# Performance work log

Hardware: AMD Instinct MI355X
Metric: run time of the kernel (lower is better)

## Reference

```python
import jax, jax.numpy as jnp
import numpy as np

B, N, DIM = 4, 1024, 1024
HEADS, DH = 16, 64
INNER = HEADS * DH          # 1024
PROJ_H = max(16, DH // 8)   # 16
TOP_K = 256
TEMP = 1.0
SCALE = DH ** -0.5
LN_EPS = 1e-5


def setup_inputs() -> dict:
    key = jax.random.key(0)
    ks = jax.random.split(key, 9)
    s = 0.02
    return {
        "x": jax.random.normal(ks[0], (B, N, DIM), dtype=jnp.float32),
        "w_qkv": jax.random.normal(ks[1], (3 * INNER, DIM), dtype=jnp.float32) * s,
        "w_out": jax.random.normal(ks[2], (DIM, INNER), dtype=jnp.float32) * s,
        "b_out": jnp.zeros((DIM,), dtype=jnp.float32),
        "ln_g": jnp.ones((DH,), dtype=jnp.float32),
        "ln_b": jnp.zeros((DH,), dtype=jnp.float32),
        "w1": jax.random.normal(ks[3], (PROJ_H, DH), dtype=jnp.float32) * s,
        "b1": jnp.zeros((PROJ_H,), dtype=jnp.float32),
        "w2": jax.random.normal(ks[4], (1, PROJ_H), dtype=jnp.float32) * s,
        "b2": jnp.zeros((1,), dtype=jnp.float32),
    }


def _soma_gate(token_feat, ln_g, ln_b, w1, b1, w2, b2):
    # token_feat: [B, N, DH] -> gate [B, N] in (0,1)
    mu = token_feat.mean(axis=-1, keepdims=True)
    var = token_feat.var(axis=-1, keepdims=True)
    H = (token_feat - mu) * jax.lax.rsqrt(var + LN_EPS) * ln_g + ln_b
    h = jax.nn.gelu(H @ w1.T + b1, approximate=False)
    scores = (h @ w2.T + b2)[..., 0]                       # [B, N]
    scores = scores / (TEMP + 1e-12)
    # top-k soft mask: non-topk positions set to -1e9 before sigmoid
    topk_vals, topk_idx = jax.lax.top_k(scores, TOP_K)
    b_idx = jnp.arange(scores.shape[0])[:, None]
    scores = jnp.full_like(scores, -1e9).at[b_idx, topk_idx].set(topk_vals)
    return jax.nn.sigmoid(scores)


def reference(x, w_qkv, w_out, b_out, ln_g, ln_b, w1, b1, w2, b2):
    Bx, Nx, _ = x.shape
    qkv = x @ w_qkv.T                                      # [B, N, 3*INNER]
    q, k, v = jnp.split(qkv, 3, axis=-1)
    to_heads = lambda t: t.reshape(Bx, Nx, HEADS, DH).transpose(0, 2, 1, 3)
    q, k, v = to_heads(q), to_heads(k), to_heads(v)        # [B, H, N, DH]

    dots = jnp.einsum('bhid,bhjd->bhij', q, k) * SCALE     # [B, H, N, N]

    q_mean = q.mean(axis=1)                                # [B, N, DH]
    gate = _soma_gate(q_mean, ln_g, ln_b, w1, b1, w2, b2)  # [B, N]
    dots = dots * (gate[:, None, :, None] * gate[:, None, None, :])

    attn = jax.nn.softmax(dots, axis=-1)
    out = jnp.einsum('bhij,bhjd->bhid', attn, v)           # [B, H, N, DH]
    out = out.transpose(0, 2, 1, 3).reshape(Bx, Nx, INNER)
    return out @ w_out.T + b_out
```

## Files before the change

### kernel.cpp

```cpp
#include <hip/hip_runtime.h>
#include <hip/hip_bf16.h>
#include <stdint.h>

typedef __bf16 bf16;
typedef __bf16 bf16x8 __attribute__((ext_vector_type(8)));
typedef float floatx4 __attribute__((ext_vector_type(4)));

typedef const __attribute__((address_space(1))) uint32_t glb_u32;
typedef __attribute__((address_space(3))) uint32_t lds_u32;

__device__ __forceinline__ void cp16(void* lds, const void* gp) {
    __builtin_amdgcn_global_load_lds((glb_u32*)gp, (lds_u32*)lds, 16, 0, 0);
}

#define MFMA16(a, b, c) __builtin_amdgcn_mfma_f32_16x16x32_bf16((a), (b), (c), 0, 0, 0)
#define SCALE_ 0.125f

__global__ __launch_bounds__(256) void k_cvt_prep(
    const float* __restrict__ x, const float* __restrict__ wq,
    const float* __restrict__ wo, bf16* __restrict__ xb,
    bf16* __restrict__ xl, bf16* __restrict__ wqb, bf16* __restrict__ wob,
    bf16* __restrict__ whl) {
    if (blockIdx.x < 4096) {
        size_t i8 = ((size_t)blockIdx.x * 256 + threadIdx.x) * 8;
        const float* src; bf16* dst; size_t off; bool isx = false;
        if (i8 < 4194304)      { src = x;  dst = xb;  off = i8; isx = true; }
        else if (i8 < 7340032) { src = wq; dst = wqb; off = i8 - 4194304; }
        else                   { src = wo; dst = wob; off = i8 - 7340032; }
        float4 a = *(const float4*)(src + off);
        float4 b = *(const float4*)(src + off + 4);
        union { bf16 h[8]; uint4 u; } hi, lo;
        hi.h[0] = (bf16)a.x; hi.h[1] = (bf16)a.y; hi.h[2] = (bf16)a.z; hi.h[3] = (bf16)a.w;
        hi.h[4] = (bf16)b.x; hi.h[5] = (bf16)b.y; hi.h[6] = (bf16)b.z; hi.h[7] = (bf16)b.w;
        *(uint4*)(dst + off) = hi.u;
        if (isx) {
            lo.h[0] = (bf16)(a.x - (float)hi.h[0]);
            lo.h[1] = (bf16)(a.y - (float)hi.h[1]);
            lo.h[2] = (bf16)(a.z - (float)hi.h[2]);
            lo.h[3] = (bf16)(a.w - (float)hi.h[3]);
            lo.h[4] = (bf16)(b.x - (float)hi.h[4]);
            lo.h[5] = (bf16)(b.y - (float)hi.h[5]);
            lo.h[6] = (bf16)(b.z - (float)hi.h[6]);
            lo.h[7] = (bf16)(b.w - (float)hi.h[7]);
            *(uint4*)(xl + off) = lo.u;
        }
    } else {
        int t = (blockIdx.x - 4096) * 256 + threadIdx.x;
        int k = t & 1023, d = t >> 10;
        float s = 0.f;
        #pragma unroll
        for (int h = 0; h < 16; ++h) s += wq[(size_t)(h * 64 + d) * 1024 + k];
        s *= (1.f / 16.f);
        bf16 hi = (bf16)s;
        whl[(size_t)d * 1024 + k] = hi;
        whl[(size_t)(64 + d) * 1024 + k] = (bf16)(s - (float)hi);
    }
}

__global__ __launch_bounds__(256) void k_score_gemm(
    const bf16* __restrict__ xh, const bf16* __restrict__ xl,
    const bf16* __restrict__ whl, float* __restrict__ qmbuf) {
    __shared__ bf16 Ah[128 * 32];
    __shared__ bf16 Al[128 * 32];
    __shared__ bf16 Bs[128 * 32];
    const int t = threadIdx.x;
    const int lane = t & 63;
    const int w = t >> 6;
    const int m0 = blockIdx.x * 128;
    const int srow = t >> 2;
    const int scol = (t & 3) * 8;
    const int fr = lane & 15;
    const int kc = (lane >> 4) * 8;
    const int wm0 = w * 32;

    floatx4 zero4 = {0.f, 0.f, 0.f, 0.f};
    floatx4 acc[2][4];
    #pragma unroll
    for (int i = 0; i < 2; ++i)
        #pragma unroll
        for (int j = 0; j < 4; ++j) acc[i][j] = zero4;

    for (int k0 = 0; k0 < 1024; k0 += 32) {
        __syncthreads();
        cp16(Ah + t * 8,        xh + (size_t)(m0 + srow) * 1024 + k0 + scol);
        cp16(Ah + t * 8 + 2048, xh + (size_t)(m0 + srow + 64) * 1024 + k0 + scol);
        cp16(Al + t * 8,        xl + (size_t)(m0 + srow) * 1024 + k0 + scol);
        cp16(Al + t * 8 + 2048, xl + (size_t)(m0 + srow + 64) * 1024 + k0 + scol);
        cp16(Bs + t * 8,        whl + (size_t)srow * 1024 + k0 + scol);
        cp16(Bs + t * 8 + 2048, whl + (size_t)(srow + 64) * 1024 + k0 + scol);
        __syncthreads();
        bf16x8 ah[2], al[2], bh[4], bl[4];
        #pragma unroll
        for (int mi = 0; mi < 2; ++mi) {
            ah[mi] = *(const bf16x8*)&Ah[(wm0 + mi * 16 + fr) * 32 + kc];
            al[mi] = *(const bf16x8*)&Al[(wm0 + mi * 16 + fr) * 32 + kc];
        }
        #pragma unroll
        for (int ni = 0; ni < 4; ++ni) {
            bh[ni] = *(const bf16x8*)&Bs[(ni * 16 + fr) * 32 + kc];
            bl[ni] = *(const bf16x8*)&Bs[(64 + ni * 16 + fr) * 32 + kc];
        }
        #pragma unroll
        for (int mi = 0; mi < 2; ++mi)
            #pragma unroll
            for (int ni = 0; ni < 4; ++ni) {
                acc[mi][ni] = MFMA16(ah[mi], bh[ni], acc[mi][ni]);
                acc[mi][ni] = MFMA16(ah[mi], bl[ni], acc[mi][ni]);
                acc[mi][ni] = MFMA16(al[mi], bh[ni], acc[mi][ni]);
            }
    }

    const int rowb = (lane >> 4) * 4;
    #pragma unroll
    for (int mi = 0; mi < 2; ++mi)
        #pragma unroll
        for (int ni = 0; ni < 4; ++ni)
            #pragma unroll
            for (int r = 0; r < 4; ++r) {
                const int row = m0 + wm0 + mi * 16 + rowb + r;
                qmbuf[(size_t)row * 64 + ni * 16 + fr] = acc[mi][ni][r];
            }
}

__global__ __launch_bounds__(256) void k_score_tail(
    const float* __restrict__ qmbuf, const float* __restrict__ lng,
    const float* __restrict__ lnb, const float* __restrict__ w1f,
    const float* __restrict__ b1f, const float* __restrict__ w2f,
    const float* __restrict__ b2f, float* __restrict__ scores) {
    const int w = threadIdx.x >> 6, lane = threadIdx.x & 63;
    const int r = blockIdx.x * 4 + w;
    __shared__ float Hs[4][64];
    __shared__ float hh[4][16];

    float qm = qmbuf[(size_t)r * 64 + lane];
    float s = qm;
    #pragma unroll
    for (int off = 32; off > 0; off >>= 1) s += __shfl_xor(s, off);
    float mu = s * (1.f / 64.f);
    float dx = qm - mu;
    float v2 = dx * dx;
    #pragma unroll
    for (int off = 32; off > 0; off >>= 1) v2 += __shfl_xor(v2, off);
    float var = v2 * (1.f / 64.f);
    float H = dx * (1.0f / sqrtf(var + 1e-5f)) * lng[lane] + lnb[lane];
    Hs[w][lane] = H;
    if (lane < 16) {
        float a = b1f[lane];
        #pragma unroll
        for (int d = 0; d < 64; ++d) a += Hs[w][d] * w1f[lane * 64 + d];
        hh[w][lane] = 0.5f * a * (1.0f + erff(a * 0.70710678118654752f));
    }
    if (lane == 0) {
        float sc = b2f[0];
        #pragma unroll
        for (int p = 0; p < 16; ++p) sc += hh[w][p] * w2f[p];
        scores[r] = sc;
    }
}

__global__ __launch_bounds__(256) void k_topk(const float* __restrict__ scores,
                                              float* __restrict__ gate,
                                              int* __restrict__ idx,
                                              float* __restrict__ gsel) {
    const int w = threadIdx.x >> 6, lane = threadIdx.x & 63;
    const float* sc = scores + w * 1024;
    float s[16];
    uint32_t key[16];
    #pragma unroll
    for (int i = 0; i < 16; ++i) {
        s[i] = sc[lane * 16 + i];
        uint32_t u = __float_as_uint(s[i]);
        key[i] = (u >> 31) ? ~u : (u | 0x80000000u);
    }
    uint32_t prefix = 0;
    for (int bit = 31; bit >= 0; --bit) {
        uint32_t cand = prefix | (1u << bit);
        int c = 0;
        #pragma unroll
        for (int i = 0; i < 16; ++i) c += (key[i] >= cand);
        #pragma unroll
        for (int off = 1; off < 64; off <<= 1) c += __shfl_xor(c, off);
        if (c >= 256) prefix = cand;
    }
    int cg = 0, eq = 0;
    #pragma unroll
    for (int i = 0; i < 16; ++i) { cg += (key[i] > prefix); eq += (key[i] == prefix); }
    #pragma unroll
    for (int off = 1; off < 64; off <<= 1) cg += __shfl_xor(cg, off);
    const int quota = 256 - cg;
    int xs = eq;
    #pragma unroll
    for (int off = 1; off < 64; off <<= 1) {
        int y = __shfl_up(xs, off);
        if (lane >= off) xs += y;
    }
    int run = xs - eq;
    bool selv[16];
    int cnt = 0;
    #pragma unroll
    for (int i = 0; i < 16; ++i) {
        bool sel = key[i] > prefix;
        if (key[i] == prefix) { sel = (run < quota); run++; }
        selv[i] = sel;
        cnt += sel ? 1 : 0;
        gate[w * 1024 + lane * 16 + i] = sel ? 1.0f / (1.0f + expf(-s[i])) : 0.0f;
    }
    int xc = cnt;
    #pragma unroll
    for (int off = 1; off < 64; off <<= 1) {
        int y = __shfl_up(xc, off);
        if (lane >= off) xc += y;
    }
    int pos = xc - cnt;
    #pragma unroll
    for (int i = 0; i < 16; ++i) {
        if (selv[i]) {
            idx[w * 256 + pos]  = lane * 16 + i;
            gsel[w * 256 + pos] = 1.0f / (1.0f + expf(-s[i]));
            pos++;
        }
    }
}

__global__ __launch_bounds__(256) void k_xsum(const bf16* __restrict__ xb,
                                              float* __restrict__ xsum4) {
    const int i = blockIdx.x;
    const int nq = i & 3, b = (i >> 2) & 3, c0 = (i >> 4) << 6;
    const int lane = threadIdx.x & 63, q = threadIdx.x >> 6;
    __shared__ float red[4][64];
    const bf16* p = xb + (size_t)b * 1048576 +
                    (size_t)(nq * 256 + q * 64) * 1024 + c0 + lane;
    float s = 0.f;
    #pragma unroll 8
    for (int n = 0; n < 64; ++n) s += (float)p[(size_t)n * 1024];
    red[q][lane] = s;
    __syncthreads();
    if (threadIdx.x < 64)
        xsum4[((size_t)nq * 4 + b) * 1024 + c0 + threadIdx.x] =
            red[0][threadIdx.x] + red[1][threadIdx.x] +
            red[2][threadIdx.x] + red[3][threadIdx.x];
}

__global__ __launch_bounds__(256) void k_qkv_sel(
    const bf16* __restrict__ xb, const bf16* __restrict__ wqb,
    const int* __restrict__ idx, bf16* __restrict__ qsel,
    bf16* __restrict__ ksel, bf16* __restrict__ VselT) {
    __shared__ bf16 As[128 * 32];
    __shared__ bf16 Bs[128 * 32];
    const int t = threadIdx.x;
    const int lane = t & 63;
    const int w = t >> 6;
    const int srow = t >> 2;
    const int scol = (t & 3) * 8;
    const int wm = (w & 1) * 64;
    const int wn = (w >> 1) * 64;
    const int fr = lane & 15;
    const int kc = (lane >> 4) * 8;

    const int bid = blockIdx.x;
    const int n0 = (bid % 24) * 128;
    const int m0 = (bid / 24) * 128;
    const bf16* Bsrc = wqb + (size_t)n0 * 1024;
    const int mg1 = m0 + srow, mg2 = mg1 + 64;
    const int tok1 = idx[(mg1 >> 8) * 256 + (mg1 & 255)];
    const int tok2 = idx[(mg2 >> 8) * 256 + (mg2 & 255)];
    const size_t abase1 = ((size_t)(mg1 >> 8) * 1024 + tok1) * 1024;
    const size_t abase2 = ((size_t)(mg2 >> 8) * 1024 + tok2) * 1024;

    floatx4 zero4 = {0.f, 0.f, 0.f, 0.f};
    floatx4 acc[4][4];
    #pragma unroll
    for (int i = 0; i < 4; ++i)
        #pragma unroll
        for (int j = 0; j < 4; ++j) acc[i][j] = zero4;

    for (int k0 = 0; k0 < 1024; k0 += 32) {
        __syncthreads();
        cp16(As + t * 8,        xb + abase1 + k0 + scol);
        cp16(As + t * 8 + 2048, xb + abase2 + k0 + scol);
        cp16(Bs + t * 8,        Bsrc + (size_t)srow * 1024 + k0 + scol);
        cp16(Bs + t * 8 + 2048, Bsrc + (size_t)(srow + 64) * 1024 + k0 + scol);
        __syncthreads();
        bf16x8 a[4], b[4];
        #pragma unroll
        for (int mi = 0; mi < 4; ++mi)
            a[mi] = *(const bf16x8*)&As[(wm + mi * 16 + fr) * 32 + kc];
        #pragma unroll
        for (int ni = 0; ni < 4; ++ni)
            b[ni] = *(const bf16x8*)&Bs[(wn + ni * 16 + fr) * 32 + kc];
        #pragma unroll
        for (int mi = 0; mi < 4; ++mi)
            #pragma unroll
            for (int ni = 0; ni < 4; ++ni)
                acc[mi][ni] = MFMA16(a[mi], b[ni], acc[mi][ni]);
    }

    const int rowb = (lane >> 4) * 4;
    #pragma unroll
    for (int ni = 0; ni < 4; ++ni) {
        const int n_base = n0 + wn + ni * 16;
        const int region = n_base >> 10;
        const int nn = n_base & 1023;
        const int h = nn >> 6;
        const int dd = (nn & 63) + fr;
        if (region < 2) {
            #pragma unroll
            for (int mi = 0; mi < 4; ++mi)
                #pragma unroll
                for (int r = 0; r < 4; ++r) {
                    const int mg = m0 + wm + mi * 16 + rowb + r;
                    const bf16 v = (bf16)acc[mi][ni][r];
                    if (region == 0) {
                        qsel[(size_t)mg * 1024 + h * 64 + dd] = v;
                    } else {
                        const int b = mg >> 8, s = mg & 255;
                        ksel[(((size_t)(b * 16 + h)) * 256 + s) * 64 + dd] = v;
                    }
                }
        } else {
            #pragma unroll
            for (int mi = 0; mi < 4; ++mi) {
                const int mgb = m0 + wm + mi * 16 + rowb;
                const int b = mgb >> 8, s0 = mgb & 255;
                union { bf16 h4[4]; uint2 u; } pk;
                #pragma unroll
                for (int r = 0; r < 4; ++r) pk.h4[r] = (bf16)acc[mi][ni][r];
                *(uint2*)&VselT[(((size_t)(b * 16 + h)) * 64 + dd) * 256 + s0] = pk.u;
            }
        }
    }
}

__global__ __launch_bounds__(256) void k_sumv(
    const float* __restrict__ xsum4, const bf16* __restrict__ wqb,
    const bf16* __restrict__ VselT, float* __restrict__ SumVuns,
    bf16* __restrict__ qsel) {
    const int bh = blockIdx.x, b = bh >> 4, h = bh & 15;
    const int t = threadIdx.x, d = t & 63, part = t >> 6;
    __shared__ float xs[1024];
    __shared__ float redA[4][64];
    __shared__ float redS[4][64];

    for (int k = t; k < 1024; k += 256)
        xs[k] = xsum4[(size_t)(0 * 4 + b) * 1024 + k] +
                xsum4[(size_t)(1 * 4 + b) * 1024 + k] +
                xsum4[(size_t)(2 * 4 + b) * 1024 + k] +
                xsum4[(size_t)(3 * 4 + b) * 1024 + k];
    __syncthreads();

    const bf16* wrow = wqb + (size_t)(2048 + h * 64 + d) * 1024 + part * 256;
    float sa = 0.f;
    #pragma unroll
    for (int k = 0; k < 256; k += 8) {
        bf16x8 v = *(const bf16x8*)(wrow + k);
        #pragma unroll
        for (int j = 0; j < 8; ++j) sa += (float)v[j] * xs[part * 256 + k + j];
    }
    redA[part][d] = sa;

    const bf16* vrow = VselT + (size_t)bh * 16384 + (size_t)d * 256 + part * 64;
    float ss = 0.f;
    #pragma unroll
    for (int k = 0; k < 64; k += 8) {
        bf16x8 v = *(const bf16x8*)(vrow + k);
        #pragma unroll
        for (int j = 0; j < 8; ++j) ss += (float)v[j];
    }
    redS[part][d] = ss;
    __syncthreads();

    if (t < 64) {
        float sA = redA[0][t] + redA[1][t] + redA[2][t] + redA[3][t];
        float sS = redS[0][t] + redS[1][t] + redS[2][t] + redS[3][t];
        SumVuns[bh * 64 + t] = sA - sS;
        qsel[(size_t)(1024 + b) * 1024 + h * 64 + t] = (bf16)(sA * (1.f / 1024.f));
    }
}

__global__ __launch_bounds__(256) void k_attn(
    bf16* __restrict__ qsel, const bf16* __restrict__ Ksel,
    const bf16* __restrict__ VselT, const float* __restrict__ gsel,
    const float* __restrict__ SumVuns) {
    const int bh = blockIdx.x;
    const int qt = blockIdx.y;
    const int b = bh >> 4, h = bh & 15;
    const int t = threadIdx.x, w = t >> 6, lane = t & 63;
    const int m0 = qt * 64;
    const bf16* kb = Ksel + (size_t)bh * 16384;
    const bf16* vb = VselT + (size_t)bh * 16384;

    __shared__ bf16 Qs[64 * 72];
    __shared__ bf16 Ks[64 * 72];
    __shared__ bf16 Vs[64 * 72];
    __shared__ bf16 Ps[4][16 * 72];

    #pragma unroll
    for (int c = 0; c < 2; ++c) {
        int idx2 = t + 256 * c, row = idx2 >> 3, c8 = (idx2 & 7) * 8;
        *(uint4*)&Qs[row * 72 + c8] =
            *(const uint4*)&qsel[(size_t)(b * 256 + m0 + row) * 1024 + h * 64 + c8];
    }
    const int fr = lane & 15;
    const int kq = lane >> 4;
    const int rowb = kq * 4;
    __syncthreads();
    bf16x8 aq[2];
    aq[0] = *(const bf16x8*)&Qs[(w * 16 + fr) * 72 + kq * 8];
    aq[1] = *(const bf16x8*)&Qs[(w * 16 + fr) * 72 + 32 + kq * 8];

    float gq[4];
    #pragma unroll
    for (int r = 0; r < 4; ++r)
        gq[r] = gsel[b * 256 + m0 + w * 16 + rowb + r] * SCALE_;

    float mrow[4] = {0.f, 0.f, 0.f, 0.f};
    float lrow[4] = {0.f, 0.f, 0.f, 0.f};
    floatx4 zero4 = {0.f, 0.f, 0.f, 0.f};
    floatx4 Of[4] = {zero4, zero4, zero4, zero4};

    for (int jt = 0; jt < 4; ++jt) {
        const int j0 = jt * 64;
        __syncthreads();
        #pragma unroll
        for (int c = 0; c < 2; ++c) {
            int idx2 = t + 256 * c, row = idx2 >> 3, c8 = (idx2 & 7) * 8;
            *(uint4*)&Ks[row * 72 + c8] = *(const uint4*)&kb[(size_t)(j0 + row) * 64 + c8];
            *(uint4*)&Vs[row * 72 + c8] = *(const uint4*)&vb[(size_t)row * 256 + j0 + c8];
        }
        __syncthreads();

        floatx4 S[4] = {zero4, zero4, zero4, zero4};
        #pragma unroll
        for (int ks = 0; ks < 2; ++ks) {
            #pragma unroll
            for (int ni = 0; ni < 4; ++ni) {
                bf16x8 bfr = *(const bf16x8*)&Ks[(ni * 16 + fr) * 72 + ks * 32 + kq * 8];
                S[ni] = MFMA16(aq[ks], bfr, S[ni]);
            }
        }
        float gk[4];
        #pragma unroll
        for (int ni = 0; ni < 4; ++ni) gk[ni] = gsel[b * 256 + j0 + ni * 16 + fr];

        float p[4][4], rmax[4] = {0.f, 0.f, 0.f, 0.f};
        #pragma unroll
        for (int ni = 0; ni < 4; ++ni)
            #pragma unroll
            for (int r = 0; r < 4; ++r) {
                float sv = S[ni][r] * (gq[r] * gk[ni]);
                p[ni][r] = sv;
                rmax[r] = fmaxf(rmax[r], sv);
            }
        #pragma unroll
        for (int r = 0; r < 4; ++r) {
            #pragma unroll
            for (int off = 1; off < 16; off <<= 1)
                rmax[r] = fmaxf(rmax[r], __shfl_xor(rmax[r], off));
        }
        float alpha[4], rsum[4] = {0.f, 0.f, 0.f, 0.f};
        #pragma unroll
        for (int r = 0; r < 4; ++r) {
            float mn = fmaxf(mrow[r], rmax[r]);
            alpha[r] = __expf(mrow[r] - mn);
            mrow[r] = mn;
        }
        #pragma unroll
        for (int ni = 0; ni < 4; ++ni)
            #pragma unroll
            for (int r = 0; r < 4; ++r) {
                float pv = __expf(p[ni][r] - mrow[r]);
                p[ni][r] = pv;
                rsum[r] += pv;
            }
        #pragma unroll
        for (int r = 0; r < 4; ++r) {
            #pragma unroll
            for (int off = 1; off < 16; off <<= 1) rsum[r] += __shfl_xor(rsum[r], off);
            lrow[r] = lrow[r] * alpha[r] + rsum[r];
        }
        #pragma unroll
        for (int nd = 0; nd < 4; ++nd)
            #pragma unroll
            for (int r = 0; r < 4; ++r) Of[nd][r] *= alpha[r];

        #pragma unroll
        for (int ni = 0; ni < 4; ++ni)
            #pragma unroll
            for (int r = 0; r < 4; ++r)
                Ps[w][(rowb + r) * 72 + ni * 16 + fr] = (bf16)p[ni][r];

        #pragma unroll
        for (int ks = 0; ks < 2; ++ks) {
            bf16x8 ap = *(const bf16x8*)&Ps[w][fr * 72 + ks * 32 + kq * 8];
            #pragma unroll
            for (int nd = 0; nd < 4; ++nd) {
                bf16x8 bv = *(const bf16x8*)&Vs[(nd * 16 + fr) * 72 + ks * 32 + kq * 8];
                Of[nd] = MFMA16(ap, bv, Of[nd]);
            }
        }
    }

    #pragma unroll
    for (int nd = 0; nd < 4; ++nd)
        #pragma unroll
        for (int r = 0; r < 4; ++r) {
            float em = __expf(-mrow[r]);
            float num = Of[nd][r] + em * SumVuns[bh * 64 + nd * 16 + fr];
            float den = lrow[r] + 768.0f * em;
            qsel[(size_t)(b * 256 + m0 + w * 16 + rowb + r) * 1024 +
                 h * 64 + nd * 16 + fr] = (bf16)(num / den);
        }
}

__global__ __launch_bounds__(256) void k_out_sel(
    const bf16* __restrict__ A, const bf16* __restrict__ wob,
    const float* __restrict__ b_out, const int* __restrict__ idx,
    float* __restrict__ ubase, float* __restrict__ out) {
    __shared__ bf16 As[128 * 32];
    __shared__ bf16 Bs[128 * 32];
    const int t = threadIdx.x;
    const int lane = t & 63;
    const int w = t >> 6;
    const int n0 = blockIdx.x * 128;
    const int m0 = blockIdx.y * 128;
    const bf16* Bsrc = wob + (size_t)n0 * 1024;

    const int srow = t >> 2;
    const int scol = (t & 3) * 8;
    const int wm = (w & 1) * 64;
    const int wn = (w >> 1) * 64;
    const int fr = lane & 15;
    const int kc = (lane >> 4) * 8;

    floatx4 zero4 = {0.f, 0.f, 0.f, 0.f};
    floatx4 acc[4][4];
    #pragma unroll
    for (int i = 0; i < 4; ++i)
        #pragma unroll
        for (int j = 0; j < 4; ++j) acc[i][j] = zero4;

    for (int k0 = 0; k0 < 1024; k0 += 32) {
        __syncthreads();
        cp16(As + t * 8,        A + (size_t)(m0 + srow) * 1024 + k0 + scol);
        cp16(As + t * 8 + 2048, A + (size_t)(m0 + srow + 64) * 1024 + k0 + scol);
        cp16(Bs + t * 8,        Bsrc + (size_t)srow * 1024 + k0 + scol);
        cp16(Bs + t * 8 + 2048, Bsrc + (size_t)(srow + 64) * 1024 + k0 + scol);
        __syncthreads();
        bf16x8 a[4], b[4];
        #pragma unroll
        for (int mi = 0; mi < 4; ++mi)
            a[mi] = *(const bf16x8*)&As[(wm + mi * 16 + fr) * 32 + kc];
        #pragma unroll
        for (int ni = 0; ni < 4; ++ni)
            b[ni] = *(const bf16x8*)&Bs[(wn + ni * 16 + fr) * 32 + kc];
        #pragma unroll
        for (int mi = 0; mi < 4; ++mi)
            #pragma unroll
            for (int ni = 0; ni < 4; ++ni)
                acc[mi][ni] = MFMA16(a[mi], b[ni], acc[mi][ni]);
    }

    const int rowb = (lane >> 4) * 4;
    #pragma unroll
    for (int ni = 0; ni < 4; ++ni) {
        const int ng = n0 + wn + ni * 16 + fr;
        const float bias = b_out[ng];
        #pragma unroll
        for (int mi = 0; mi < 4; ++mi)
            #pragma unroll
            for (int r = 0; r < 4; ++r) {
                const int mg = m0 + wm + mi * 16 + rowb + r;
                const float val = acc[mi][ni][r] + bias;
                if (mg < 1024) {
                    const int b = mg >> 8, s = mg & 255;
                    const int tok = idx[b * 256 + s];
                    out[((size_t)b * 1024 + tok) * 1024 + ng] = val;
                } else if (mg < 1028) {
                    ubase[(size_t)(mg - 1024) * 1024 + ng] = val;
                }
            }
    }
}

__global__ __launch_bounds__(256) void k_fill(
    const float* __restrict__ gate, const float* __restrict__ ubase,
    float* __restrict__ out) {
    const int tokg = blockIdx.x;
    if (gate[tokg] > 0.f) return;
    const int b = tokg >> 10;
    const int c = threadIdx.x * 4;
    *(float4*)(out + (size_t)tokg * 1024 + c) = *(const float4*)(ubase + b * 1024 + c);
}

extern "C" void kernel_launch(void* const* d_in, const int* in_sizes, int n_in,
                              void* d_out, int out_size, void* d_ws, size_t ws_size,
                              hipStream_t stream) {
    const float* x     = (const float*)d_in[0];
    const float* w_qkv = (const float*)d_in[1];
    const float* w_out = (const float*)d_in[2];
    const float* b_out = (const float*)d_in[3];
    const float* ln_g  = (const float*)d_in[4];
    const float* ln_b  = (const float*)d_in[5];
    const float* w1    = (const float*)d_in[6];
    const float* b1    = (const float*)d_in[7];
    const float* w2    = (const float*)d_in[8];
    const float* b2    = (const float*)d_in[9];
    float* out = (float*)d_out;

    char* ws = (char*)d_ws;
    bf16*  qsel  = (bf16*)(ws);
    bf16*  ksel  = (bf16*)(ws + 4194304);
    bf16*  VselT = (bf16*)(ws + 6291456);
    float* xsum4 = (float*)(ws + 8388608);
    bf16*  xb    = (bf16*)(ws + 16777216);
    bf16*  wqb   = (bf16*)(ws + 25165824);
    bf16*  wob   = (bf16*)(ws + 31457280);
    int*   idx     = (int*)(ws + 33554432);
    float* gsel    = (float*)(ws + 33558528);
    float* scores  = (float*)(ws + 33562624);
    float* gate    = (float*)(ws + 33579008);
    float* SumVuns = (float*)(ws + 33595392);
    float* ubase   = (float*)(ws + 33611776);
    bf16*  whl     = (bf16*)(ws + 33685504);
    float* qmbuf   = (float*)(ws + 34603008);
    bf16*  xlbuf   = (bf16*)(ws + 35651584);

    k_cvt_prep<<<4352, 256, 0, stream>>>(x, w_qkv, w_out, xb, xlbuf, wqb, wob, whl);
    k_xsum<<<256, 256, 0, stream>>>(xb, xsum4);
    k_score_gemm<<<32, 256, 0, stream>>>(xb, xlbuf, whl, qmbuf);
    k_score_tail<<<1024, 256, 0, stream>>>(qmbuf, ln_g, ln_b, w1, b1, w2, b2, scores);
    k_topk<<<1, 256, 0, stream>>>(scores, gate, idx, gsel);
    k_qkv_sel<<<192, 256, 0, stream>>>(xb, wqb, idx, qsel, ksel, VselT);
    k_sumv<<<64, 256, 0, stream>>>(xsum4, wqb, VselT, SumVuns, qsel);
    k_attn<<<dim3(64, 4), 256, 0, stream>>>(qsel, ksel, VselT, gsel, SumVuns);
    k_out_sel<<<dim3(8, 9), 256, 0, stream>>>(qsel, wob, b_out, idx, ubase, out);
    k_fill<<<4096, 256, 0, stream>>>(gate, ubase, out);
}
```

Baseline: 225.4 us.

## Fuse auxiliary kernels into neighbors to cut launch count from ten to six

Folds the column-sum of x into the conversion kernel, reading fp32 x directly. The score tail (LayerNorm, MLP, GELU) moves into the score GEMM epilogue through shared memory. The mean-V projection and the ubase output row become extra blocks inside the qkv and attention kernels, and the fill pass becomes extra blocks of the output GEMM. Intent is to remove launch and serialization overhead and intermediate buffer round-trips. In exchange the sum-over-V reduction is recomputed per attention block, and some blocks are unbalanced or sequential, such as the 32-row serial loop in the GEMM epilogue.

Result: slower. 240.1 us (+6.5%).

```diff
diff --git a/kernel.cpp b/kernel.cpp
--- a/kernel.cpp
+++ b/kernel.cpp
@@ -20,7 +20,8 @@
     const float* __restrict__ x, const float* __restrict__ wq,
     const float* __restrict__ wo, bf16* __restrict__ xb,
     bf16* __restrict__ xl, bf16* __restrict__ wqb, bf16* __restrict__ wob,
-    bf16* __restrict__ whl) {
+    bf16* __restrict__ whl, float* __restrict__ xsum) {
+    __shared__ float red[4][64];
     if (blockIdx.x < 4096) {
         size_t i8 = ((size_t)blockIdx.x * 256 + threadIdx.x) * 8;
         const float* src; bf16* dst; size_t off; bool isx = false;
@@ -44,7 +45,7 @@
             lo.h[7] = (bf16)(b.w - (float)hi.h[7]);
             *(uint4*)(xl + off) = lo.u;
         }
-    } else {
+    } else if (blockIdx.x < 4352) {
         int t = (blockIdx.x - 4096) * 256 + threadIdx.x;
         int k = t & 1023, d = t >> 10;
         float s = 0.f;
@@ -54,15 +55,34 @@
         bf16 hi = (bf16)s;
         whl[(size_t)d * 1024 + k] = hi;
         whl[(size_t)(64 + d) * 1024 + k] = (bf16)(s - (float)hi);
+    } else {
+        int j = blockIdx.x - 4352;
+        int b = j >> 4, c0 = (j & 15) << 6;
+        int lane = threadIdx.x & 63, q = threadIdx.x >> 6;
+        const float* p = x + (size_t)b * 1048576 + (size_t)q * 262144 + c0 + lane;
+        float s = 0.f;
+        #pragma unroll 8
+        for (int n = 0; n < 256; ++n) s += p[(size_t)n * 1024];
+        red[q][lane] = s;
+        __syncthreads();
+        if (threadIdx.x < 64)
+            xsum[b * 1024 + c0 + threadIdx.x] =
+                red[0][threadIdx.x] + red[1][threadIdx.x] +
+                red[2][threadIdx.x] + red[3][threadIdx.x];
     }
 }
 
 __global__ __launch_bounds__(256) void k_score_gemm(
     const bf16* __restrict__ xh, const bf16* __restrict__ xl,
-    const bf16* __restrict__ whl, float* __restrict__ qmbuf) {
+    const bf16* __restrict__ whl, const float* __restrict__ lng,
+    const float* __restrict__ lnb, const float* __restrict__ w1f,
+    const float* __restrict__ b1f, const float* __restrict__ w2f,
+    const float* __restrict__ b2f, float* __restrict__ scores) {
     __shared__ bf16 Ah[128 * 32];
     __shared__ bf16 Al[128 * 32];
     __shared__ bf16 Bs[128 * 32];
+    __shared__ float Sbuf[128][65];
+    __shared__ float Hs[4][64];
     const int t = threadIdx.x;
     const int lane = t & 63;
     const int w = t >> 6;
@@ -116,45 +136,41 @@
         #pragma unroll
         for (int ni = 0; ni < 4; ++ni)
             #pragma unroll
-            for (int r = 0; r < 4; ++r) {
-                const int row = m0 + wm0 + mi * 16 + rowb + r;
-                qmbuf[(size_t)row * 64 + ni * 16 + fr] = acc[mi][ni][r];
-            }
-}
-
-__global__ __launch_bounds__(256) void k_score_tail(
-    const float* __restrict__ qmbuf, const float* __restrict__ lng,
-    const float* __restrict__ lnb, const float* __restrict__ w1f,
-    const float* __restrict__ b1f, const float* __restrict__ w2f,
-    const float* __restrict__ b2f, float* __restrict__ scores) {
-    const int w = threadIdx.x >> 6, lane = threadIdx.x & 63;
-    const int r = blockIdx.x * 4 + w;
-    __shared__ float Hs[4][64];
-    __shared__ float hh[4][16];
-
-    float qm = qmbuf[(size_t)r * 64 + lane];
-    float s = qm;
-    #pragma unroll
-    for (int off = 32; off > 0; off >>= 1) s += __shfl_xor(s, off);
-    float mu = s * (1.f / 64.f);
-    float dx = qm - mu;
-    float v2 = dx * dx;
-    #pragma unroll
-    for (int off = 32; off > 0; off >>= 1) v2 += __shfl_xor(v2, off);
-    float var = v2 * (1.f / 64.f);
-    float H = dx * (1.0f / sqrtf(var + 1e-5f)) * lng[lane] + lnb[lane];
-    Hs[w][lane] = H;
-    if (lane < 16) {
-        float a = b1f[lane];
-        #pragma unroll
-        for (int d = 0; d < 64; ++d) a += Hs[w][d] * w1f[lane * 64 + d];
-        hh[w][lane] = 0.5f * a * (1.0f + erff(a * 0.70710678118654752f));
-    }
-    if (lane == 0) {
-        float sc = b2f[0];
-        #pragma unroll
-        for (int p = 0; p < 16; ++p) sc += hh[w][p] * w2f[p];
-        scores[r] = sc;
+            for (int r = 0; r < 4; ++r)
+                Sbuf[wm0 + mi * 16 + rowb + r][ni * 16 + fr] = acc[mi][ni][r];
+
+    const int p = lane & 15, q = lane >> 4;
+    float w1r[16];
+    #pragma unroll
+    for (int j = 0; j < 16; ++j) w1r[j] = w1f[p * 64 + q * 16 + j];
+    const float b1r = b1f[p], w2r = w2f[p], b2r = b2f[0];
+    const float lgr = lng[lane], lbr = lnb[lane];
+    __syncthreads();
+    for (int rr = 0; rr < 32; ++rr) {
+        const int row = w * 32 + rr;
+        float qm = Sbuf[row][lane];
+        float s = qm;
+        #pragma unroll
+        for (int off = 32; off > 0; off >>= 1) s += __shfl_xor(s, off);
+        float mu = s * (1.f / 64.f);
+        float dx = qm - mu;
+        float v2 = dx * dx;
+        #pragma unroll
+        for (int off = 32; off > 0; off >>= 1) v2 += __shfl_xor(v2, off);
+        float var = v2 * (1.f / 64.f);
+        float H = dx * (1.0f / sqrtf(var + 1e-5f)) * lgr + lbr;
+        Hs[w][lane] = H;
+        float pa = 0.f;
+        #pragma unroll
+        for (int j = 0; j < 16; ++j) pa += Hs[w][q * 16 + j] * w1r[j];
+        pa += __shfl_xor(pa, 16);
+        pa += __shfl_xor(pa, 32);
+        float a = pa + b1r;
+        float g = 0.5f * a * (1.0f + erff(a * 0.70710678118654752f));
+        float sc = g * w2r;
+        #pragma unroll
+        for (int off = 1; off < 16; off <<= 1) sc += __shfl_xor(sc, off);
+        if (lane == 0) scores[m0 + row] = sc + b2r;
     }
 }
 
@@ -222,32 +238,32 @@
     }
 }
 
-__global__ __launch_bounds__(256) void k_xsum(const bf16* __restrict__ xb,
-                                              float* __restrict__ xsum4) {
-    const int i = blockIdx.x;
-    const int nq = i & 3, b = (i >> 2) & 3, c0 = (i >> 4) << 6;
-    const int lane = threadIdx.x & 63, q = threadIdx.x >> 6;
-    __shared__ float red[4][64];
-    const bf16* p = xb + (size_t)b * 1048576 +
-                    (size_t)(nq * 256 + q * 64) * 1024 + c0 + lane;
-    float s = 0.f;
-    #pragma unroll 8
-    for (int n = 0; n < 64; ++n) s += (float)p[(size_t)n * 1024];
-    red[q][lane] = s;
-    __syncthreads();
-    if (threadIdx.x < 64)
-        xsum4[((size_t)nq * 4 + b) * 1024 + c0 + threadIdx.x] =
-            red[0][threadIdx.x] + red[1][threadIdx.x] +
-            red[2][threadIdx.x] + red[3][threadIdx.x];
-}
-
 __global__ __launch_bounds__(256) void k_qkv_sel(
     const bf16* __restrict__ xb, const bf16* __restrict__ wqb,
     const int* __restrict__ idx, bf16* __restrict__ qsel,
-    bf16* __restrict__ ksel, bf16* __restrict__ VselT) {
+    bf16* __restrict__ ksel, bf16* __restrict__ VselT,
+    const float* __restrict__ xsum, float* __restrict__ meanVbuf) {
     __shared__ bf16 As[128 * 32];
     __shared__ bf16 Bs[128 * 32];
+    __shared__ float xsS[1024];
     const int t = threadIdx.x;
+
+    if (blockIdx.x >= 192) {
+        const int j = blockIdx.x - 192, b = j >> 2, kq = j & 3;
+        for (int k = t; k < 1024; k += 256) xsS[k] = xsum[b * 1024 + k];
+        __syncthreads();
+        const int k2 = kq * 256 + t;
+        const bf16* wr = wqb + (size_t)(2048 + k2) * 1024;
+        float s = 0.f;
+        for (int k = 0; k < 1024; k += 8) {
+            bf16x8 v = *(const bf16x8*)(wr + k);
+            #pragma unroll
+            for (int jj = 0; jj < 8; ++jj) s += (float)v[jj] * xsS[k + jj];
+        }
+        meanVbuf[b * 1024 + k2] = s * (1.f / 1024.f);
+        return;
+    }
+
     const int lane = t & 63;
     const int w = t >> 6;
     const int srow = t >> 2;
@@ -331,68 +347,43 @@
     }
 }
 
-__global__ __launch_bounds__(256) void k_sumv(
-    const float* __restrict__ xsum4, const bf16* __restrict__ wqb,
-    const bf16* __restrict__ VselT, float* __restrict__ SumVuns,
-    bf16* __restrict__ qsel) {
-    const int bh = blockIdx.x, b = bh >> 4, h = bh & 15;
-    const int t = threadIdx.x, d = t & 63, part = t >> 6;
-    __shared__ float xs[1024];
-    __shared__ float redA[4][64];
-    __shared__ float redS[4][64];
-
-    for (int k = t; k < 1024; k += 256)
-        xs[k] = xsum4[(size_t)(0 * 4 + b) * 1024 + k] +
-                xsum4[(size_t)(1 * 4 + b) * 1024 + k] +
-                xsum4[(size_t)(2 * 4 + b) * 1024 + k] +
-                xsum4[(size_t)(3 * 4 + b) * 1024 + k];
-    __syncthreads();
-
-    const bf16* wrow = wqb + (size_t)(2048 + h * 64 + d) * 1024 + part * 256;
-    float sa = 0.f;
-    #pragma unroll
-    for (int k = 0; k < 256; k += 8) {
-        bf16x8 v = *(const bf16x8*)(wrow + k);
-        #pragma unroll
-        for (int j = 0; j < 8; ++j) sa += (float)v[j] * xs[part * 256 + k + j];
-    }
-    redA[part][d] = sa;
-
-    const bf16* vrow = VselT + (size_t)bh * 16384 + (size_t)d * 256 + part * 64;
-    float ss = 0.f;
-    #pragma unroll
-    for (int k = 0; k < 64; k += 8) {
-        bf16x8 v = *(const bf16x8*)(vrow + k);
-        #pragma unroll
-        for (int j = 0; j < 8; ++j) ss += (float)v[j];
-    }
-    redS[part][d] = ss;
-    __syncthreads();
-
-    if (t < 64) {
-        float sA = redA[0][t] + redA[1][t] + redA[2][t] + redA[3][t];
-        float sS = redS[0][t] + redS[1][t] + redS[2][t] + redS[3][t];
-        SumVuns[bh * 64 + t] = sA - sS;
-        qsel[(size_t)(1024 + b) * 1024 + h * 64 + t] = (bf16)(sA * (1.f / 1024.f));
-    }
-}
-
 __global__ __launch_bounds__(256) void k_attn(
     bf16* __restrict__ qsel, const bf16* __restrict__ Ksel,
     const bf16* __restrict__ VselT, const float* __restrict__ gsel,
-    const float* __restrict__ SumVuns) {
-    const int bh = blockIdx.x;
-    const int qt = blockIdx.y;
-    const int b = bh >> 4, h = bh & 15;
-    const int t = threadIdx.x, w = t >> 6, lane = t & 63;
-    const int m0 = qt * 64;
-    const bf16* kb = Ksel + (size_t)bh * 16384;
-    const bf16* vb = VselT + (size_t)bh * 16384;
-
+    const float* __restrict__ meanVbuf, const bf16* __restrict__ wob,
+    const float* __restrict__ b_out, float* __restrict__ ubase) {
     __shared__ bf16 Qs[64 * 72];
     __shared__ bf16 Ks[64 * 72];
     __shared__ bf16 Vs[64 * 72];
     __shared__ bf16 Ps[4][16 * 72];
+    __shared__ float redS[4][64];
+    __shared__ float SumV[64];
+    __shared__ float mvS[1024];
+    const int t = threadIdx.x;
+
+    if (blockIdx.x >= 256) {
+        const int j = blockIdx.x - 256, bb = j >> 2, nq = j & 3;
+        for (int k = t; k < 1024; k += 256) mvS[k] = meanVbuf[bb * 1024 + k];
+        __syncthreads();
+        const int n = nq * 256 + t;
+        const bf16* wr = wob + (size_t)n * 1024;
+        float s = b_out[n];
+        for (int k = 0; k < 1024; k += 8) {
+            bf16x8 v = *(const bf16x8*)(wr + k);
+            #pragma unroll
+            for (int jj = 0; jj < 8; ++jj) s += (float)v[jj] * mvS[k + jj];
+        }
+        ubase[bb * 1024 + n] = s;
+        return;
+    }
+
+    const int bh = blockIdx.x >> 2;
+    const int qt = blockIdx.x & 3;
+    const int b = bh >> 4, h = bh & 15;
+    const int w = t >> 6, lane = t & 63;
+    const int m0 = qt * 64;
+    const bf16* kb = Ksel + (size_t)bh * 16384;
+    const bf16* vb = VselT + (size_t)bh * 16384;
 
     #pragma unroll
     for (int c = 0; c < 2; ++c) {
@@ -400,10 +391,25 @@
         *(uint4*)&Qs[row * 72 + c8] =
             *(const uint4*)&qsel[(size_t)(b * 256 + m0 + row) * 1024 + h * 64 + c8];
     }
+    {
+        const int dd_ = t & 63, pp_ = t >> 6;
+        const bf16* vr = vb + (size_t)dd_ * 256 + pp_ * 64;
+        float ss = 0.f;
+        #pragma unroll
+        for (int k = 0; k < 64; k += 8) {
+            bf16x8 v = *(const bf16x8*)(vr + k);
+            #pragma unroll
+            for (int jj = 0; jj < 8; ++jj) ss += (float)v[jj];
+        }
+        redS[pp_][dd_] = ss;
+    }
     const int fr = lane & 15;
     const int kq = lane >> 4;
     const int rowb = kq * 4;
     __syncthreads();
+    if (t < 64)
+        SumV[t] = meanVbuf[b * 1024 + h * 64 + t] * 1024.f -
+                  (redS[0][t] + redS[1][t] + redS[2][t] + redS[3][t]);
     bf16x8 aq[2];
     aq[0] = *(const bf16x8*)&Qs[(w * 16 + fr) * 72 + kq * 8];
     aq[1] = *(const bf16x8*)&Qs[(w * 16 + fr) * 72 + 32 + kq * 8];
@@ -505,7 +511,7 @@
         #pragma unroll
         for (int r = 0; r < 4; ++r) {
             float em = __expf(-mrow[r]);
-            float num = Of[nd][r] + em * SumVuns[bh * 64 + nd * 16 + fr];
+            float num = Of[nd][r] + em * SumV[nd * 16 + fr];
             float den = lrow[r] + 768.0f * em;
             qsel[(size_t)(b * 256 + m0 + w * 16 + rowb + r) * 1024 +
                  h * 64 + nd * 16 + fr] = (bf16)(num / den);
@@ -515,14 +521,31 @@
 __global__ __launch_bounds__(256) void k_out_sel(
     const bf16* __restrict__ A, const bf16* __restrict__ wob,
     const float* __restrict__ b_out, const int* __restrict__ idx,
-    float* __restrict__ ubase, float* __restrict__ out) {
+    const float* __restrict__ ubase, const float* __restrict__ gate,
+    float* __restrict__ out) {
     __shared__ bf16 As[128 * 32];
     __shared__ bf16 Bs[128 * 32];
     const int t = threadIdx.x;
+    const int gb = blockIdx.x;
+
+    if (gb >= 64) {
+        const int fb = gb - 64;
+        const int c = t * 4;
+        #pragma unroll
+        for (int r = 0; r < 4; ++r) {
+            const int tokg = fb * 4 + r;
+            if (gate[tokg] > 0.f) continue;
+            const int b = tokg >> 10;
+            *(float4*)(out + (size_t)tokg * 1024 + c) =
+                *(const float4*)(ubase + b * 1024 + c);
+        }
+        return;
+    }
+
     const int lane = t & 63;
     const int w = t >> 6;
-    const int n0 = blockIdx.x * 128;
-    const int m0 = blockIdx.y * 128;
+    const int n0 = (gb & 7) * 128;
+    const int m0 = (gb >> 3) * 128;
     const bf16* Bsrc = wob + (size_t)n0 * 1024;
 
     const int srow = t >> 2;
@@ -571,25 +594,11 @@
             for (int r = 0; r < 4; ++r) {
                 const int mg = m0 + wm + mi * 16 + rowb + r;
                 const float val = acc[mi][ni][r] + bias;
-                if (mg < 1024) {
-                    const int b = mg >> 8, s = mg & 255;
-                    const int tok = idx[b * 256 + s];
-                    out[((size_t)b * 1024 + tok) * 1024 + ng] = val;
-                } else if (mg < 1028) {
-                    ubase[(size_t)(mg - 1024) * 1024 + ng] = val;
-                }
+                const int bb = mg >> 8, ss = mg & 255;
+                const int tok = idx[bb * 256 + ss];
+                out[((size_t)bb * 1024 + tok) * 1024 + ng] = val;
             }
     }
-}
-
-__global__ __launch_bounds__(256) void k_fill(
-    const float* __restrict__ gate, const float* __restrict__ ubase,
-    float* __restrict__ out) {
-    const int tokg = blockIdx.x;
-    if (gate[tokg] > 0.f) return;
-    const int b = tokg >> 10;
-    const int c = threadIdx.x * 4;
-    *(float4*)(out + (size_t)tokg * 1024 + c) = *(const float4*)(ubase + b * 1024 + c);
 }
 
 extern "C" void kernel_launch(void* const* d_in, const int* in_sizes, int n_in,
@@ -611,28 +620,23 @@
     bf16*  qsel  = (bf16*)(ws);
     bf16*  ksel  = (bf16*)(ws + 4194304);
     bf16*  VselT = (bf16*)(ws + 6291456);
-    float* xsum4 = (float*)(ws + 8388608);
+    float* xsum  = (float*)(ws + 8388608);
     bf16*  xb    = (bf16*)(ws + 16777216);
     bf16*  wqb   = (bf16*)(ws + 25165824);
     bf16*  wob   = (bf16*)(ws + 31457280);
-    int*   idx     = (int*)(ws + 33554432);
-    float* gsel    = (float*)(ws + 33558528);
-    float* scores  = (float*)(ws + 33562624);
-    float* gate    = (float*)(ws + 33579008);
-    float* SumVuns = (float*)(ws + 33595392);
-    float* ubase   = (float*)(ws + 33611776);
-    bf16*  whl     = (bf16*)(ws + 33685504);
-    float* qmbuf   = (float*)(ws + 34603008);
-    bf16*  xlbuf   = (bf16*)(ws + 35651584);
-
-    k_cvt_prep<<<4352, 256, 0, stream>>>(x, w_qkv, w_out, xb, xlbuf, wqb, wob, whl);
-    k_xsum<<<256, 256, 0, stream>>>(xb, xsum4);
-    k_score_gemm<<<32, 256, 0, stream>>>(xb, xlbuf, whl, qmbuf);
-    k_score_tail<<<1024, 256, 0, stream>>>(qmbuf, ln_g, ln_b, w1, b1, w2, b2, scores);
+    int*   idx      = (int*)(ws + 33554432);
+    float* gsel     = (float*)(ws + 33558528);
+    float* scores   = (float*)(ws + 33562624);
+    float* gate     = (float*)(ws + 33579008);
+    float* meanVbuf = (float*)(ws + 33595392);
+    float* ubase    = (float*)(ws + 33611776);
+    bf16*  whl      = (bf16*)(ws + 33685504);
+    bf16*  xlbuf    = (bf16*)(ws + 35651584);
+
+    k_cvt_prep<<<4416, 256, 0, stream>>>(x, w_qkv, w_out, xb, xlbuf, wqb, wob, whl, xsum);
+    k_score_gemm<<<32, 256, 0, stream>>>(xb, xlbuf, whl, ln_g, ln_b, w1, b1, w2, b2, scores);
     k_topk<<<1, 256, 0, stream>>>(scores, gate, idx, gsel);
-    k_qkv_sel<<<192, 256, 0, stream>>>(xb, wqb, idx, qsel, ksel, VselT);
-    k_sumv<<<64, 256, 0, stream>>>(xsum4, wqb, VselT, SumVuns, qsel);
-    k_attn<<<dim3(64, 4), 256, 0, stream>>>(qsel, ksel, VselT, gsel, SumVuns);
-    k_out_sel<<<dim3(8, 9), 256, 0, stream>>>(qsel, wob, b_out, idx, ubase, out);
-    k_fill<<<4096, 256, 0, stream>>>(gate, ubase, out);
-}
+    k_qkv_sel<<<208, 256, 0, stream>>>(xb, wqb, idx, qsel, ksel, VselT, xsum, meanVbuf);
+    k_attn<<<272, 256, 0, stream>>>(qsel, ksel, VselT, gsel, meanVbuf, wob, b_out, ubase);
+    k_out_sel<<<1088, 256, 0, stream>>>(qsel, wob, b_out, idx, ubase, gate, out);
+}
```
